# Kernel optimization log

Hardware: AMD Instinct MI355X
Metric: run time of the kernel (lower is better)

Reference implementation:

```python
import jax, jax.numpy as jnp
import numpy as np

NUM_IN_CH = 64
DIM = 256
HEADS = 8


def conv1x1(x, w):
    # x: [b,c,h,w], w: [o,c,1,1] -> [b,o,h,w]
    return jnp.einsum('bchw,oc->bohw', x, w[:, :, 0, 0])


def dwconv3(x, w):
    # depthwise 3x3, padding=1; w: [c,1,3,3]
    return jax.lax.conv_general_dilated(
        x, w, window_strides=(1, 1), padding='SAME',
        feature_group_count=x.shape[1],
        dimension_numbers=('NCHW', 'OIHW', 'NCHW'))


def setup_inputs() -> dict:
    key = jax.random.key(0)
    ks = jax.random.split(key, 12)
    B, C, H, W = 8, NUM_IN_CH, 128, 128
    s = 0.02
    return {
        'x': jax.random.normal(ks[0], (B, C, H, W), jnp.float32),
        'y': jax.random.normal(ks[1], (B, C, H, W), jnp.float32),
        'z': jax.random.normal(ks[2], (B, C, H, W), jnp.float32),
        'Wq': jax.random.normal(ks[3], (DIM, C, 1, 1), jnp.float32) * s,
        'Wq_dw': jax.random.normal(ks[4], (DIM, 1, 3, 3), jnp.float32) * s,
        'Wk': jax.random.normal(ks[5], (DIM, C, 1, 1), jnp.float32) * s,
        'Wk_dw': jax.random.normal(ks[6], (DIM, 1, 3, 3), jnp.float32) * s,
        'Wv': jax.random.normal(ks[7], (DIM, C, 1, 1), jnp.float32) * s,
        'Wv_dw': jax.random.normal(ks[8], (DIM, 1, 3, 3), jnp.float32) * s,
        'Wproj': jax.random.normal(ks[9], (DIM, DIM, 1, 1), jnp.float32) * s,
        'Wfus': jax.random.normal(ks[10], (DIM, 3 * C, 1, 1), jnp.float32) * s,
        'temperature': jnp.ones((HEADS, 1, 1), jnp.float32),
    }


def reference(x, y, z, Wq, Wq_dw, Wk, Wk_dw, Wv, Wv_dw, Wproj, Wfus, temperature):
    b, c, h, w = x.shape
    hw = h * w
    q = dwconv3(conv1x1(x, Wq), Wq_dw)
    k = dwconv3(conv1x1(y, Wk), Wk_dw)
    v = dwconv3(conv1x1(z, Wv), Wv_dw)
    f = conv1x1(jnp.concatenate([x, y, z], axis=1), Wfus)

    def to_heads(t):  # [b, dim, h, w] -> [b, head, c_head, hw]
        return t.reshape(b, HEADS, DIM // HEADS, hw)

    q, k, v = to_heads(q), to_heads(k), to_heads(v)
    # L2-normalize over the spatial (hw) axis, eps matches torch F.normalize
    qn = q / jnp.maximum(jnp.sqrt(jnp.sum(q * q, axis=-1, keepdims=True)), 1e-12)
    kn = k / jnp.maximum(jnp.sqrt(jnp.sum(k * k, axis=-1, keepdims=True)), 1e-12)
    attn = jnp.einsum('bhcn,bhdn->bhcd', qn, kn) * temperature  # [b,head,c,c]
    attn = jax.nn.softmax(attn, axis=-1)
    out = jnp.einsum('bhcd,bhdn->bhcn', attn, v).reshape(b, DIM, h, w)
    out = conv1x1(out, Wproj)
    return out + f
```

## Files before the change

### kernel.cpp

```cpp
#include <hip/hip_runtime.h>
#include <cstdint>

#define B_   8
#define CIN  64
#define DIM_ 256
#define H_   128
#define W_   128
#define HW_  (H_*W_)

typedef unsigned short u16;
typedef unsigned int   u32;
typedef short short8 __attribute__((ext_vector_type(8)));
typedef float f32x4  __attribute__((ext_vector_type(4)));

__device__ __forceinline__ u16 f2bf(float f) {
    u32 u = __float_as_uint(f);
    u32 r = (u + 0x7fffu + ((u >> 16) & 1u)) >> 16;
    return (u16)r;
}
__device__ __forceinline__ float bf2f(u16 h) {
    return __uint_as_float(((u32)h) << 16);
}

__global__ __launch_bounds__(256) void conv_mfma_kernel(
    const float* __restrict__ in, const float* __restrict__ Wc,
    u16* __restrict__ pre)
{
    __shared__ u16 Alds[256 * 64];
    __shared__ u16 Blds[128 * 64];

    const int tid = threadIdx.x;
    const int b = blockIdx.y;
    const int px0 = blockIdx.x * 128;

    {
        const int row = tid;
        const float* wp = Wc + (size_t)row * 64;
        #pragma unroll
        for (int s = 0; s < 8; ++s) {
            float4 f0 = *(const float4*)(wp + s * 8);
            float4 f1 = *(const float4*)(wp + s * 8 + 4);
            uint4 pk;
            pk.x = f2bf(f0.x) | ((u32)f2bf(f0.y) << 16);
            pk.y = f2bf(f0.z) | ((u32)f2bf(f0.w) << 16);
            pk.z = f2bf(f1.x) | ((u32)f2bf(f1.y) << 16);
            pk.w = f2bf(f1.z) | ((u32)f2bf(f1.w) << 16);
            *(uint4*)&Alds[row * 64 + ((s * 8) ^ ((row & 7) << 3))] = pk;
        }
    }
    #pragma unroll
    for (int v4 = 0; v4 < 4; ++v4) {
        int it = tid + v4 * 256;
        int px = it & 127, cg = it >> 7;
        const float* sp = in + ((size_t)b * CIN + cg * 8) * HW_ + px0 + px;
        u32 wv[4];
        #pragma unroll
        for (int j = 0; j < 4; ++j) {
            float a = sp[(size_t)(2 * j) * HW_];
            float c = sp[(size_t)(2 * j + 1) * HW_];
            wv[j] = f2bf(a) | ((u32)f2bf(c) << 16);
        }
        *(uint4*)&Blds[px * 64 + ((cg * 8) ^ ((px & 7) << 3))] =
            make_uint4(wv[0], wv[1], wv[2], wv[3]);
    }
    __syncthreads();

    const int lane = tid & 63, wid = tid >> 6;
    const int g = lane >> 4, ln = lane & 15;
    const int m0 = wid * 64;
    f32x4 acc[4][8] = {};

    #pragma unroll
    for (int ks = 0; ks < 2; ++ks) {
        short8 af[4];
        #pragma unroll
        for (int fm = 0; fm < 4; ++fm) {
            int m = m0 + fm * 16 + ln;
            af[fm] = *(const short8*)&Alds[m * 64 + ((ks * 32 + g * 8) ^ ((m & 7) << 3))];
        }
        #pragma unroll
        for (int fn = 0; fn < 8; ++fn) {
            int p = fn * 16 + ln;
            short8 bf = *(const short8*)&Blds[p * 64 + ((ks * 32 + g * 8) ^ ((p & 7) << 3))];
            #pragma unroll
            for (int fm = 0; fm < 4; ++fm)
                acc[fm][fn] = __builtin_amdgcn_mfma_f32_16x16x32_bf16(af[fm], bf, acc[fm][fn], 0, 0, 0);
        }
    }

    u16* op = pre + (size_t)b * DIM_ * HW_;
    #pragma unroll
    for (int fm = 0; fm < 4; ++fm)
        #pragma unroll
        for (int fn = 0; fn < 8; ++fn)
            #pragma unroll
            for (int r = 0; r < 4; ++r) {
                int ch = m0 + fm * 16 + g * 4 + r;
                op[(size_t)ch * HW_ + px0 + fn * 16 + ln] = f2bf(acc[fm][fn][r]);
            }
}

__global__ __launch_bounds__(256) void dw_kernel(
    const u16* __restrict__ pre, const float* __restrict__ Wd,
    u16* __restrict__ dst)
{
    __shared__ u16 t0[34][144];

    const int tid = threadIdx.x;
    const int y0 = blockIdx.x * 32;
    const int ch = blockIdx.y;
    const int b = blockIdx.z;
    const u16* src = pre + ((size_t)b * DIM_ + ch) * HW_;

    for (int i = tid; i < 68; i += 256)
        t0[i >> 1][(i & 1) ? 136 : 7] = 0;
    for (int i = tid; i < 544; i += 256) {
        int row = i >> 4, seg = i & 15;
        int gy = y0 - 1 + row;
        uint4 v = make_uint4(0, 0, 0, 0);
        if (gy >= 0 && gy < H_) v = *(const uint4*)(src + (size_t)gy * W_ + seg * 8);
        *(uint4*)&t0[row][8 + seg * 8] = v;
    }
    const float* wv = Wd + (size_t)ch * 9;
    float w00 = wv[0], w01 = wv[1], w02 = wv[2];
    float w10 = wv[3], w11 = wv[4], w12 = wv[5];
    float w20 = wv[6], w21 = wv[7], w22 = wv[8];
    __syncthreads();

    const int px = tid & 127, half = tid >> 7;
    u16* op = dst + ((size_t)b * DIM_ + ch) * HW_;
    float h0m2 = 0.f, h0m1 = 0.f, h1m1 = 0.f;
    #pragma unroll
    for (int y = 0; y < 18; ++y) {
        int r = half * 16 + y;
        float v0 = bf2f(t0[r][7 + px]);
        float v1 = bf2f(t0[r][8 + px]);
        float v2 = bf2f(t0[r][9 + px]);
        float h0 = fmaf(v0, w00, fmaf(v1, w01, v2 * w02));
        float h1 = fmaf(v0, w10, fmaf(v1, w11, v2 * w12));
        float h2 = fmaf(v0, w20, fmaf(v1, w21, v2 * w22));
        if (y >= 2)
            op[(size_t)(y0 + half * 16 + y - 2) * W_ + px] = f2bf(h0m2 + h1m1 + h2);
        h0m2 = h0m1; h0m1 = h0; h1m1 = h1;
    }
}

__global__ __launch_bounds__(256) void gram_mfma_kernel(
    const u16* __restrict__ q, const u16* __restrict__ k,
    float* __restrict__ pgram, float* __restrict__ pssq, float* __restrict__ pssk)
{
    __shared__ float red[4][1024];
    __shared__ float redq[4][32];
    __shared__ float redk[4][32];

    const int bh = blockIdx.y;
    const int chunk = blockIdx.x;
    const int tid = threadIdx.x;
    const int lane = tid & 63, wid = tid >> 6;
    const int g = lane >> 4, ln = lane & 15;

    const size_t off = (size_t)(bh * 32 + ln) * HW_ + chunk * 2048 + wid * 512 + g * 8;
    const u16* qp = q + off;
    const u16* kp = k + off;

    f32x4 aqk[2][2] = {};
    f32x4 aqq[2] = {};
    f32x4 akk[2] = {};

    #pragma unroll 4
    for (int n = 0; n < 512; n += 32) {
        short8 qf[2], kf[2];
        qf[0] = *(const short8*)(qp + n);
        qf[1] = *(const short8*)(qp + (size_t)16 * HW_ + n);
        kf[0] = *(const short8*)(kp + n);
        kf[1] = *(const short8*)(kp + (size_t)16 * HW_ + n);
        #pragma unroll
        for (int ti = 0; ti < 2; ++ti)
            #pragma unroll
            for (int tj = 0; tj < 2; ++tj)
                aqk[ti][tj] = __builtin_amdgcn_mfma_f32_16x16x32_bf16(qf[ti], kf[tj], aqk[ti][tj], 0, 0, 0);
        #pragma unroll
        for (int ti = 0; ti < 2; ++ti) {
            aqq[ti] = __builtin_amdgcn_mfma_f32_16x16x32_bf16(qf[ti], qf[ti], aqq[ti], 0, 0, 0);
            akk[ti] = __builtin_amdgcn_mfma_f32_16x16x32_bf16(kf[ti], kf[ti], akk[ti], 0, 0, 0);
        }
    }

    #pragma unroll
    for (int ti = 0; ti < 2; ++ti)
        #pragma unroll
        for (int tj = 0; tj < 2; ++tj)
            #pragma unroll
            for (int r = 0; r < 4; ++r)
                red[wid][(ti * 16 + g * 4 + r) * 32 + tj * 16 + ln] = aqk[ti][tj][r];
    if ((ln >> 2) == g) {
        #pragma unroll
        for (int ti = 0; ti < 2; ++ti) {
            redq[wid][ti * 16 + ln] = aqq[ti][ln & 3];
            redk[wid][ti * 16 + ln] = akk[ti][ln & 3];
        }
    }
    __syncthreads();

    for (int p = tid; p < 1024; p += 256) {
        float s = red[0][p] + red[1][p] + red[2][p] + red[3][p];
        pgram[((size_t)bh * 8 + chunk) * 1024 + p] = s;
    }
    if (tid < 32) {
        pssq[((size_t)bh * 8 + chunk) * 32 + tid] =
            redq[0][tid] + redq[1][tid] + redq[2][tid] + redq[3][tid];
    } else if (tid < 64) {
        int j = tid & 31;
        pssk[((size_t)bh * 8 + chunk) * 32 + j] =
            redk[0][j] + redk[1][j] + redk[2][j] + redk[3][j];
    }
}

__global__ __launch_bounds__(256) void softproj_kernel(
    const float* __restrict__ pgram, const float* __restrict__ pssq,
    const float* __restrict__ pssk, const float* __restrict__ Wproj,
    const float* __restrict__ temp, u16* __restrict__ Amm)
{
    __shared__ float att[32][33];
    __shared__ float nq[32], nk[32];

    const int bh = blockIdx.x;
    const int h = bh & 7;
    const int b = bh >> 3;
    const int tid = threadIdx.x;

    for (int p = tid; p < 1024; p += 256) {
        float s = 0.f;
        #pragma unroll
        for (int c = 0; c < 8; ++c) s += pgram[((size_t)bh * 8 + c) * 1024 + p];
        att[p >> 5][p & 31] = s;
    }
    if (tid < 32) {
        float s = 0.f;
        #pragma unroll
        for (int c = 0; c < 8; ++c) s += pssq[((size_t)bh * 8 + c) * 32 + tid];
        nq[tid] = fmaxf(sqrtf(s), 1e-12f);
    } else if (tid < 64) {
        int i = tid & 31;
        float s = 0.f;
        #pragma unroll
        for (int c = 0; c < 8; ++c) s += pssk[((size_t)bh * 8 + c) * 32 + i];
        nk[i] = fmaxf(sqrtf(s), 1e-12f);
    }
    __syncthreads();

    const float T = temp[h];
    if (tid < 32) {
        int i = tid;
        float row[32];
        float mx = -1e30f;
        float qi = T / nq[i];
        #pragma unroll
        for (int j = 0; j < 32; ++j) {
            float v = att[i][j] * qi / nk[j];
            row[j] = v;
            mx = fmaxf(mx, v);
        }
        float s = 0.f;
        #pragma unroll
        for (int j = 0; j < 32; ++j) { float e = expf(row[j] - mx); row[j] = e; s += e; }
        float inv = 1.f / s;
        #pragma unroll
        for (int j = 0; j < 32; ++j) att[i][j] = row[j] * inv;
    }
    __syncthreads();

    const int o = tid;
    float wp[32];
    #pragma unroll
    for (int i2 = 0; i2 < 32; i2 += 4)
        *(float4*)&wp[i2] = *(const float4*)&Wproj[(size_t)o * DIM_ + h * 32 + i2];
    u16* arow = Amm + ((size_t)b * DIM_ + o) * DIM_ + h * 32;
    #pragma unroll
    for (int j = 0; j < 32; ++j) {
        float s = 0.f;
        #pragma unroll
        for (int i = 0; i < 32; ++i) s = fmaf(wp[i], att[i][j], s);
        arow[j] = f2bf(s);
    }
}

__global__ __launch_bounds__(256) void wfus_cast_kernel(
    const float* __restrict__ Wfus, u16* __restrict__ Afus)
{
    int idx = blockIdx.x * 256 + threadIdx.x;
    int base = idx * 8;
    float4 f0 = *(const float4*)(Wfus + base);
    float4 f1 = *(const float4*)(Wfus + base + 4);
    uint4 pk;
    pk.x = f2bf(f0.x) | ((u32)f2bf(f0.y) << 16);
    pk.y = f2bf(f0.z) | ((u32)f2bf(f0.w) << 16);
    pk.z = f2bf(f1.x) | ((u32)f2bf(f1.y) << 16);
    pk.w = f2bf(f1.z) | ((u32)f2bf(f1.w) << 16);
    *(uint4*)(Afus + base) = pk;
}

__global__ __launch_bounds__(256, 2) void final2_kernel(
    const u16* __restrict__ Amm, const u16* __restrict__ Afus,
    const u16* __restrict__ vbuf,
    const float* __restrict__ xin, const float* __restrict__ yin,
    const float* __restrict__ zin, float* __restrict__ out)
{
    __shared__ u16 Bl[2][128 * 64];

    const int tid = threadIdx.x;
    const int b = blockIdx.y;
    const int px0 = blockIdx.x * 128;
    const int lane = tid & 63, wid = tid >> 6;
    const int g = lane >> 4, ln = lane & 15;
    const int m0 = wid * 64;

    f32x4 acc[4][8] = {};
    uint4  gq[2][4];
    float4 gx[2][8];
    short8 af[2][8];

    auto loadB = [&](int kc, uint4* q4, float4* x4) {
        if (kc < 4) {
            #pragma unroll
            for (int i = 0; i < 4; ++i) {
                int tt = i * 256 + tid;
                int r = tt >> 4, pc = tt & 15;
                q4[i] = *(const uint4*)(vbuf + ((size_t)b * DIM_ + kc * 64 + r) * HW_ + px0 + pc * 8);
            }
        } else {
            #pragma unroll
            for (int i = 0; i < 4; ++i) {
                int tt = i * 256 + tid;
                int r = tt >> 4, pc = tt & 15;
                int c = kc * 64 + r - 256;
                const float* basep = (c < 64) ? xin : (c < 128) ? yin : zin;
                const float* sp = basep + ((size_t)b * CIN + (c & 63)) * HW_ + px0 + pc * 8;
                x4[2 * i]     = *(const float4*)sp;
                x4[2 * i + 1] = *(const float4*)(sp + 4);
            }
        }
    };
    auto writeB = [&](int kc, int buf, uint4* q4, float4* x4) {
        u16* dst = &Bl[buf][0];
        #pragma unroll
        for (int i = 0; i < 4; ++i) {
            int tt = i * 256 + tid;
            int r = tt >> 4, pc = tt & 15;
            if (kc < 4) {
                #pragma unroll
                for (int e = 0; e < 4; ++e) {
                    u32 w = ((const u32*)&q4[i])[e];
                    int j0 = 2 * e, j1 = 2 * e + 1;
                    dst[(pc * 8 + j0) * 64 + (((r >> 3) ^ j0) << 3) + (r & 7)] = (u16)w;
                    dst[(pc * 8 + j1) * 64 + (((r >> 3) ^ j1) << 3) + (r & 7)] = (u16)(w >> 16);
                }
            } else {
                float f[8];
                *(float4*)&f[0] = x4[2 * i];
                *(float4*)&f[4] = x4[2 * i + 1];
                #pragma unroll
                for (int j = 0; j < 8; ++j)
                    dst[(pc * 8 + j) * 64 + (((r >> 3) ^ j) << 3) + (r & 7)] = f2bf(f[j]);
            }
        }
    };
    auto loadA = [&](int kc, short8* a8) {
        #pragma unroll
        for (int ks = 0; ks < 2; ++ks)
            #pragma unroll
            for (int fm = 0; fm < 4; ++fm) {
                int m = m0 + fm * 16 + ln;
                const u16* p = (kc < 4)
                    ? Amm + ((size_t)b * DIM_ + m) * DIM_ + kc * 64 + ks * 32 + g * 8
                    : Afus + (size_t)m * 192 + (kc - 4) * 64 + ks * 32 + g * 8;
                a8[ks * 4 + fm] = *(const short8*)p;
            }
    };

    loadB(0, gq[0], gx[0]);
    loadA(0, af[0]);
    writeB(0, 0, gq[0], gx[0]);
    __syncthreads();

    #pragma unroll
    for (int kc = 0; kc < 7; ++kc) {
        const int cur = kc & 1, nxt = cur ^ 1;
        if (kc < 6) {
            loadB(kc + 1, gq[nxt], gx[nxt]);
            loadA(kc + 1, af[nxt]);
        }
        #pragma unroll
        for (int ks = 0; ks < 2; ++ks) {
            #pragma unroll
            for (int fn = 0; fn < 8; ++fn) {
                int p = fn * 16 + ln;
                short8 bf = *(const short8*)&Bl[cur][p * 64 + ((ks * 32 + g * 8) ^ ((p & 7) << 3))];
                #pragma unroll
                for (int fm = 0; fm < 4; ++fm)
                    acc[fm][fn] = __builtin_amdgcn_mfma_f32_16x16x32_bf16(af[cur][ks * 4 + fm], bf, acc[fm][fn], 0, 0, 0);
            }
        }
        if (kc < 6) {
            writeB(kc + 1, nxt, gq[nxt], gx[nxt]);
            __syncthreads();
        }
    }

    float* op = out + (size_t)b * DIM_ * HW_;
    #pragma unroll
    for (int fm = 0; fm < 4; ++fm)
        #pragma unroll
        for (int fn = 0; fn < 8; ++fn)
            #pragma unroll
            for (int r = 0; r < 4; ++r) {
                int ch = m0 + fm * 16 + g * 4 + r;
                op[(size_t)ch * HW_ + px0 + fn * 16 + ln] = acc[fm][fn][r];
            }
}

extern "C" void kernel_launch(void* const* d_in, const int* in_sizes, int n_in,
                              void* d_out, int out_size, void* d_ws, size_t ws_size,
                              hipStream_t stream) {
    (void)in_sizes; (void)n_in; (void)out_size; (void)ws_size;

    const float* x     = (const float*)d_in[0];
    const float* y     = (const float*)d_in[1];
    const float* z     = (const float*)d_in[2];
    const float* Wq    = (const float*)d_in[3];
    const float* Wqd   = (const float*)d_in[4];
    const float* Wk    = (const float*)d_in[5];
    const float* Wkd   = (const float*)d_in[6];
    const float* Wv    = (const float*)d_in[7];
    const float* Wvd   = (const float*)d_in[8];
    const float* Wproj = (const float*)d_in[9];
    const float* Wfus  = (const float*)d_in[10];
    const float* temp  = (const float*)d_in[11];

    const size_t QELEMS = (size_t)B_ * DIM_ * HW_;

    u16* preb = (u16*)d_out;
    u16* qbuf = (u16*)d_out + QELEMS;
    u16* kvbuf = (u16*)d_ws;
    char* wsp = (char*)d_ws + QELEMS * sizeof(u16);
    float* pgram = (float*)wsp;                       wsp += 64 * 8 * 1024 * 4;
    float* pssq  = (float*)wsp;                       wsp += 64 * 8 * 32 * 4;
    float* pssk  = (float*)wsp;                       wsp += 64 * 8 * 32 * 4;
    u16*   Amm   = (u16*)wsp;                         wsp += (size_t)B_ * DIM_ * DIM_ * 2;
    u16*   Afus  = (u16*)wsp;

    dim3 cgrid(128, B_);
    dim3 dgrid(4, DIM_, B_);

    wfus_cast_kernel<<<24, 256, 0, stream>>>(Wfus, Afus);
    conv_mfma_kernel<<<cgrid, 256, 0, stream>>>(x, Wq, preb);
    dw_kernel<<<dgrid, 256, 0, stream>>>(preb, Wqd, qbuf);
    conv_mfma_kernel<<<cgrid, 256, 0, stream>>>(y, Wk, preb);
    dw_kernel<<<dgrid, 256, 0, stream>>>(preb, Wkd, kvbuf);
    gram_mfma_kernel<<<dim3(8, 64), 256, 0, stream>>>(qbuf, kvbuf, pgram, pssq, pssk);
    softproj_kernel<<<64, 256, 0, stream>>>(pgram, pssq, pssk, Wproj, temp, Amm);
    conv_mfma_kernel<<<cgrid, 256, 0, stream>>>(z, Wv, preb);
    dw_kernel<<<dgrid, 256, 0, stream>>>(preb, Wvd, kvbuf);
    final2_kernel<<<cgrid, 256, 0, stream>>>(Amm, Afus, kvbuf, x, y, z, (float*)d_out);
}
```

Before: 319.8 us.

## Split final GEMM over output-channel halves and transpose B via per-pixel gathers

```diff
diff --git a/kernel.cpp b/kernel.cpp
--- a/kernel.cpp
+++ b/kernel.cpp
@@ -300,7 +300,33 @@
     *(uint4*)(Afus + base) = pk;
 }
 
-__global__ __launch_bounds__(256, 2) void final2_kernel(
+#define LOADB_F3(KC, W) do {                                                    \
+    if ((KC) < 4) {                                                             \
+        _Pragma("unroll") for (int i_ = 0; i_ < 2; ++i_) {                      \
+            const u16* vb_ = vbuf + ((size_t)b * DIM_ + (KC) * 64 + (qq0 + 2 * i_) * 16) * HW_ + px0 + pxu; \
+            _Pragma("unroll") for (int jj_ = 0; jj_ < 8; ++jj_)                 \
+                W[i_][jj_] = (u32)vb_[(size_t)(2 * jj_) * HW_]                  \
+                           | ((u32)vb_[(size_t)(2 * jj_ + 1) * HW_] << 16);     \
+        }                                                                       \
+    } else {                                                                    \
+        const float* bp_ = ((KC) == 4) ? xin : ((KC) == 5) ? yin : zin;         \
+        _Pragma("unroll") for (int i_ = 0; i_ < 2; ++i_) {                      \
+            const float* sp_ = bp_ + ((size_t)b * CIN + (qq0 + 2 * i_) * 16) * HW_ + px0 + pxu; \
+            _Pragma("unroll") for (int jj_ = 0; jj_ < 8; ++jj_)                 \
+                W[i_][jj_] = (u32)f2bf(sp_[(size_t)(2 * jj_) * HW_])            \
+                           | ((u32)f2bf(sp_[(size_t)(2 * jj_ + 1) * HW_]) << 16); \
+        }                                                                       \
+    } } while (0)
+
+#define WRITEB_F3(BUF, W) do {                                                  \
+    u16* dd_ = &Bl[BUF][pxu * 64];                                              \
+    _Pragma("unroll") for (int i_ = 0; i_ < 2; ++i_) {                          \
+        int qq_ = qq0 + 2 * i_;                                                 \
+        *(uint4*)&dd_[(qq_ * 16)     ^ ((pxu & 7) << 3)] = make_uint4(W[i_][0], W[i_][1], W[i_][2], W[i_][3]); \
+        *(uint4*)&dd_[(qq_ * 16 + 8) ^ ((pxu & 7) << 3)] = make_uint4(W[i_][4], W[i_][5], W[i_][6], W[i_][7]); \
+    } } while (0)
+
+__global__ __launch_bounds__(256) void final3_kernel(
     const u16* __restrict__ Amm, const u16* __restrict__ Afus,
     const u16* __restrict__ vbuf,
     const float* __restrict__ xin, const float* __restrict__ yin,
@@ -309,107 +335,65 @@
     __shared__ u16 Bl[2][128 * 64];
 
     const int tid = threadIdx.x;
-    const int b = blockIdx.y;
     const int px0 = blockIdx.x * 128;
+    const int o0  = blockIdx.y * 128;
+    const int b   = blockIdx.z;
     const int lane = tid & 63, wid = tid >> 6;
     const int g = lane >> 4, ln = lane & 15;
-    const int m0 = wid * 64;
-
-    f32x4 acc[4][8] = {};
-    uint4  gq[2][4];
-    float4 gx[2][8];
-    short8 af[2][8];
-
-    auto loadB = [&](int kc, uint4* q4, float4* x4) {
-        if (kc < 4) {
-            #pragma unroll
-            for (int i = 0; i < 4; ++i) {
-                int tt = i * 256 + tid;
-                int r = tt >> 4, pc = tt & 15;
-                q4[i] = *(const uint4*)(vbuf + ((size_t)b * DIM_ + kc * 64 + r) * HW_ + px0 + pc * 8);
-            }
-        } else {
-            #pragma unroll
-            for (int i = 0; i < 4; ++i) {
-                int tt = i * 256 + tid;
-                int r = tt >> 4, pc = tt & 15;
-                int c = kc * 64 + r - 256;
-                const float* basep = (c < 64) ? xin : (c < 128) ? yin : zin;
-                const float* sp = basep + ((size_t)b * CIN + (c & 63)) * HW_ + px0 + pc * 8;
-                x4[2 * i]     = *(const float4*)sp;
-                x4[2 * i + 1] = *(const float4*)(sp + 4);
-            }
-        }
-    };
-    auto writeB = [&](int kc, int buf, uint4* q4, float4* x4) {
-        u16* dst = &Bl[buf][0];
-        #pragma unroll
-        for (int i = 0; i < 4; ++i) {
-            int tt = i * 256 + tid;
-            int r = tt >> 4, pc = tt & 15;
-            if (kc < 4) {
-                #pragma unroll
-                for (int e = 0; e < 4; ++e) {
-                    u32 w = ((const u32*)&q4[i])[e];
-                    int j0 = 2 * e, j1 = 2 * e + 1;
-                    dst[(pc * 8 + j0) * 64 + (((r >> 3) ^ j0) << 3) + (r & 7)] = (u16)w;
-                    dst[(pc * 8 + j1) * 64 + (((r >> 3) ^ j1) << 3) + (r & 7)] = (u16)(w >> 16);
-                }
-            } else {
-                float f[8];
-                *(float4*)&f[0] = x4[2 * i];
-                *(float4*)&f[4] = x4[2 * i + 1];
-                #pragma unroll
-                for (int j = 0; j < 8; ++j)
-                    dst[(pc * 8 + j) * 64 + (((r >> 3) ^ j) << 3) + (r & 7)] = f2bf(f[j]);
-            }
-        }
-    };
-    auto loadA = [&](int kc, short8* a8) {
+    const int m0 = o0 + wid * 32;
+
+    const int pxu = tid & 127;
+    const int qq0 = tid >> 7;
+
+    f32x4 acc[2][8] = {};
+
+    {
+        u32 w0[2][8];
+        LOADB_F3(0, w0);
+        WRITEB_F3(0, w0);
+    }
+    __syncthreads();
+
+    #pragma unroll
+    for (int kc = 0; kc < 7; ++kc) {
+        const int cur = kc & 1;
+
+        u32 wn[2][8];
+        if (kc < 6) {
+            LOADB_F3(kc + 1, wn);
+        }
+
+        short8 a[4];
         #pragma unroll
         for (int ks = 0; ks < 2; ++ks)
             #pragma unroll
-            for (int fm = 0; fm < 4; ++fm) {
+            for (int fm = 0; fm < 2; ++fm) {
                 int m = m0 + fm * 16 + ln;
-                const u16* p = (kc < 4)
+                const u16* ap = (kc < 4)
                     ? Amm + ((size_t)b * DIM_ + m) * DIM_ + kc * 64 + ks * 32 + g * 8
                     : Afus + (size_t)m * 192 + (kc - 4) * 64 + ks * 32 + g * 8;
-                a8[ks * 4 + fm] = *(const short8*)p;
+                a[ks * 2 + fm] = *(const short8*)ap;
             }
-    };
-
-    loadB(0, gq[0], gx[0]);
-    loadA(0, af[0]);
-    writeB(0, 0, gq[0], gx[0]);
-    __syncthreads();
-
-    #pragma unroll
-    for (int kc = 0; kc < 7; ++kc) {
-        const int cur = kc & 1, nxt = cur ^ 1;
-        if (kc < 6) {
-            loadB(kc + 1, gq[nxt], gx[nxt]);
-            loadA(kc + 1, af[nxt]);
-        }
-        #pragma unroll
-        for (int ks = 0; ks < 2; ++ks) {
+
+        #pragma unroll
+        for (int ks = 0; ks < 2; ++ks)
             #pragma unroll
             for (int fn = 0; fn < 8; ++fn) {
                 int p = fn * 16 + ln;
                 short8 bf = *(const short8*)&Bl[cur][p * 64 + ((ks * 32 + g * 8) ^ ((p & 7) << 3))];
-                #pragma unroll
-                for (int fm = 0; fm < 4; ++fm)
-                    acc[fm][fn] = __builtin_amdgcn_mfma_f32_16x16x32_bf16(af[cur][ks * 4 + fm], bf, acc[fm][fn], 0, 0, 0);
+                acc[0][fn] = __builtin_amdgcn_mfma_f32_16x16x32_bf16(a[ks * 2 + 0], bf, acc[0][fn], 0, 0, 0);
+                acc[1][fn] = __builtin_amdgcn_mfma_f32_16x16x32_bf16(a[ks * 2 + 1], bf, acc[1][fn], 0, 0, 0);
             }
-        }
+
         if (kc < 6) {
-            writeB(kc + 1, nxt, gq[nxt], gx[nxt]);
+            WRITEB_F3(cur ^ 1, wn);
             __syncthreads();
         }
     }
 
     float* op = out + (size_t)b * DIM_ * HW_;
     #pragma unroll
-    for (int fm = 0; fm < 4; ++fm)
+    for (int fm = 0; fm < 2; ++fm)
         #pragma unroll
         for (int fn = 0; fn < 8; ++fn)
             #pragma unroll
@@ -461,5 +445,5 @@
     softproj_kernel<<<64, 256, 0, stream>>>(pgram, pssq, pssk, Wproj, temp, Amm);
     conv_mfma_kernel<<<cgrid, 256, 0, stream>>>(z, Wv, preb);
     dw_kernel<<<dgrid, 256, 0, stream>>>(preb, Wvd, kvbuf);
-    final2_kernel<<<cgrid, 256, 0, stream>>>(Amm, Afus, kvbuf, x, y, z, (float*)d_out);
-}
+    final3_kernel<<<dim3(128, 2, B_), 256, 0, stream>>>(Amm, Afus, kvbuf, x, y, z, (float*)d_out);
+}
```

Result: faster. 286.3 us (-10.5%).
